# Kernel optimization log

Measured on AMD Instinct MI355X. Metric: run time of the kernel, lower is better.

Reference implementation:

```python
import jax, jax.numpy as jnp
import numpy as np

EMB_DIM = 1024
N_HEAD = 16
HEAD_DIM = EMB_DIM // N_HEAD


def setup_inputs() -> dict:
    key = jax.random.key(0)
    k1, k2, k3, k4, k5 = jax.random.split(key, 5)
    x = jax.random.normal(k1, (4, 2048, EMB_DIM), dtype=jnp.float32)
    s = 1.0 / np.sqrt(EMB_DIM)
    W_qkv = jax.random.uniform(k2, (3 * EMB_DIM, EMB_DIM), minval=-s, maxval=s, dtype=jnp.float32)
    b_qkv = jax.random.uniform(k3, (3 * EMB_DIM,), minval=-s, maxval=s, dtype=jnp.float32)
    W_proj = jax.random.uniform(k4, (EMB_DIM, EMB_DIM), minval=-s, maxval=s, dtype=jnp.float32)
    b_proj = jax.random.uniform(k5, (EMB_DIM,), minval=-s, maxval=s, dtype=jnp.float32)
    return {"x": x, "W_qkv": W_qkv, "b_qkv": b_qkv, "W_proj": W_proj, "b_proj": b_proj}


def reference(x, W_qkv, b_qkv, W_proj, b_proj):
    B, S, E = x.shape
    H, D = N_HEAD, HEAD_DIM
    qkv = x @ W_qkv.T + b_qkv  # [B,S,3E]
    q, k, v = jnp.split(qkv, 3, axis=-1)
    # [B,S,E] -> [B,H,S,D]
    q = q.reshape(B, S, H, D).transpose(0, 2, 1, 3)
    k = k.reshape(B, S, H, D).transpose(0, 2, 1, 3)
    v = v.reshape(B, S, H, D).transpose(0, 2, 1, 3)
    scale = 1.0 / jnp.sqrt(jnp.asarray(D, dtype=x.dtype))
    scores = jnp.einsum('bhqd,bhkd->bhqk', q, k) * scale
    causal = jnp.tril(jnp.ones((S, S), dtype=bool))
    scores = jnp.where(causal, scores, jnp.asarray(-jnp.inf, dtype=scores.dtype))
    attn = jax.nn.softmax(scores, axis=-1)
    y = jnp.einsum('bhqk,bhkd->bhqd', attn, v)  # [B,H,S,D]
    y = y.transpose(0, 2, 1, 3).reshape(B, S, E)
    return y @ W_proj.T + b_proj
```

## Files before the change

### kernel.cpp

```cpp
#include <hip/hip_runtime.h>
#include <hip/hip_bf16.h>

typedef __attribute__((ext_vector_type(4))) float f32x4;
typedef __attribute__((ext_vector_type(8))) __bf16 bf16x8;
typedef __attribute__((ext_vector_type(4))) unsigned int u32x4;

#define EMB 1024
#define NHEAD 16
#define HDIM 64
#define SEQ 2048
#define BATCH 4
#define NTOK 8192

__device__ __forceinline__ unsigned short f2bf(float f) {
    unsigned int u = __builtin_bit_cast(unsigned int, f);
    u = (u + 0x7fffu + ((u >> 16) & 1u)) >> 16;
    return (unsigned short)u;
}

__device__ __forceinline__ unsigned int pack_bf2(float lo, float hi) {
    unsigned int a = __builtin_bit_cast(unsigned int, lo);
    unsigned int b = __builtin_bit_cast(unsigned int, hi);
    return ((a + 0x8000u) >> 16) | ((b + 0x8000u) & 0xffff0000u);
}

__device__ __forceinline__ unsigned long long pack_bf4(const f32x4 v) {
    unsigned long long lo = pack_bf2(v[0], v[1]);
    unsigned long long hi = pack_bf2(v[2], v[3]);
    return (hi << 32) | lo;
}

__device__ __forceinline__ void async_copy16(const ushort* g, ushort* l) {
    __builtin_amdgcn_global_load_lds(
        (const __attribute__((address_space(1))) void*)g,
        (__attribute__((address_space(3))) void*)l,
        16, 0, 0);
}

__global__ void cvt_f32_bf16(const float4* __restrict__ in, ushort* __restrict__ out, int n4) {
    int i = blockIdx.x * 256 + threadIdx.x;
    if (i < n4) {
        float4 v = in[i];
        ushort4 o;
        o.x = f2bf(v.x); o.y = f2bf(v.y); o.z = f2bf(v.z); o.w = f2bf(v.w);
        ((ushort4*)out)[i] = o;
    }
}

#define GEMM_STAGE(Asrc, Bsrc, m0, n0, kt)                                        \
    {                                                                             \
        _Pragma("unroll")                                                         \
        for (int j = 0; j < 2; ++j) {                                             \
            int row = wave * 32 + j * 16 + (lane >> 2);                           \
            int kc  = (lane & 3) ^ ((row >> 1) & 3);                              \
            async_copy16(Asrc + (size_t)(m0 + row) * EMB + kt + kc * 8,           \
                         As + (wave * 32 + j * 16) * 32);                         \
            async_copy16(Bsrc + (size_t)(n0 + row) * EMB + kt + kc * 8,           \
                         Bs + (wave * 32 + j * 16) * 32);                         \
        }                                                                         \
    }

#define GEMM_BODY(Asrc, Bsrc, m0, n0)                                             \
    f32x4 acc[4][4] = {};                                                         \
    for (int kt = 0; kt < EMB; kt += 32) {                                        \
        GEMM_STAGE(Asrc, Bsrc, m0, n0, kt)                                        \
        __syncthreads();                                                          \
        bf16x8 a[4], b[4];                                                        \
        _Pragma("unroll")                                                         \
        for (int i = 0; i < 4; ++i) {                                             \
            int r = wm + i * 16 + col;                                            \
            a[i] = *(const bf16x8*)&As[r * 32 + (quad ^ ((r >> 1) & 3)) * 8];     \
            int c = wn + i * 16 + col;                                            \
            b[i] = *(const bf16x8*)&Bs[c * 32 + (quad ^ ((c >> 1) & 3)) * 8];     \
        }                                                                         \
        _Pragma("unroll")                                                         \
        for (int i = 0; i < 4; ++i)                                               \
            _Pragma("unroll")                                                     \
            for (int j = 0; j < 4; ++j)                                           \
                acc[i][j] = __builtin_amdgcn_mfma_f32_16x16x32_bf16(              \
                    a[i], b[j], acc[i][j], 0, 0, 0);                              \
        __syncthreads();                                                         \
    }

__global__ __launch_bounds__(256) void gemm_qk(
    const ushort* __restrict__ A,
    const ushort* __restrict__ W,
    const float*  __restrict__ bias,
    ushort* __restrict__ Qb, ushort* __restrict__ Kb)
{
    __shared__ ushort As[128 * 32];
    __shared__ ushort Bs[128 * 32];
    const int tid  = threadIdx.x;
    const int lane = tid & 63;
    const int wave = tid >> 6;
    const int col  = lane & 15;
    const int quad = lane >> 4;
    const int m0 = blockIdx.x * 128;
    const int n0 = blockIdx.y * 128;
    const int wm = (wave >> 1) * 64;
    const int wn = (wave & 1) * 64;

    GEMM_BODY(A, W, m0, n0)

    #pragma unroll
    for (int i = 0; i < 4; ++i)
        #pragma unroll
        for (int j = 0; j < 4; ++j)
            #pragma unroll
            for (int r = 0; r < 4; ++r) {
                int m = m0 + wm + i * 16 + quad * 4 + r;
                int n = n0 + wn + j * 16 + col;
                float v = acc[i][j][r] + bias[n];
                unsigned short bv = f2bf(v);
                int e = n & 1023;
                int h = e >> 6, d = e & 63;
                int b = m >> 11, s = m & 2047;
                size_t bh = (size_t)(b * NHEAD + h);
                if (n < 1024) Qb[(bh * SEQ + s) * HDIM + d] = bv;
                else          Kb[(bh * SEQ + s) * HDIM + d] = bv;
            }
}

__global__ __launch_bounds__(256) void gemm_vt(
    const ushort* __restrict__ Wv,
    const ushort* __restrict__ X,
    const float*  __restrict__ bias,
    ushort* __restrict__ Vtx)
{
    __shared__ ushort As[128 * 32];
    __shared__ ushort Bs[128 * 32];
    const int tid  = threadIdx.x;
    const int lane = tid & 63;
    const int wave = tid >> 6;
    const int col  = lane & 15;
    const int quad = lane >> 4;
    const int m0 = blockIdx.x * 128;
    const int n0 = blockIdx.y * 128;
    const int wm = (wave >> 1) * 64;
    const int wn = (wave & 1) * 64;

    GEMM_BODY(Wv, X, m0, n0)

    #pragma unroll
    for (int i = 0; i < 4; ++i)
        #pragma unroll
        for (int j = 0; j < 4; ++j)
            #pragma unroll
            for (int r = 0; r < 4; ++r) {
                int m = m0 + wm + i * 16 + quad * 4 + r;
                int n = n0 + wn + j * 16 + col;
                Vtx[(size_t)m * NTOK + n] = f2bf(acc[i][j][r] + bias[m]);
            }
}

__global__ __launch_bounds__(256) void gemm_proj(
    const ushort* __restrict__ A,
    const ushort* __restrict__ W,
    const float*  __restrict__ bias,
    float* __restrict__ out)
{
    __shared__ ushort As[128 * 32];
    __shared__ ushort Bs[128 * 32];
    const int tid  = threadIdx.x;
    const int lane = tid & 63;
    const int wave = tid >> 6;
    const int col  = lane & 15;
    const int quad = lane >> 4;
    const int m0 = blockIdx.x * 128;
    const int n0 = blockIdx.y * 128;
    const int wm = (wave >> 1) * 64;
    const int wn = (wave & 1) * 64;

    GEMM_BODY(A, W, m0, n0)

    #pragma unroll
    for (int i = 0; i < 4; ++i)
        #pragma unroll
        for (int j = 0; j < 4; ++j)
            #pragma unroll
            for (int r = 0; r < 4; ++r) {
                int m = m0 + wm + i * 16 + quad * 4 + r;
                int n = n0 + wn + j * 16 + col;
                out[(size_t)m * EMB + n] = acc[i][j][r] + bias[n];
            }
}

__device__ __forceinline__ void attn_qtile(
    int qb, int b, int h, int lane, int wave,
    const ushort* __restrict__ Qh, const ushort* __restrict__ Kh,
    const ushort* __restrict__ Vh, ushort* __restrict__ Yb,
    ushort* __restrict__ Ks0, ushort* __restrict__ Ks1, ushort* __restrict__ Vs,
    ushort* __restrict__ Ps)
{
    const int col  = lane & 15;
    const int quad = lane >> 4;
    const int q0  = qb * 64 + wave * 16;
    const int row = q0 + col;
    const float SC = 0.125f * 1.44269504f;

    bf16x8 qf0 = *(const bf16x8*)(Qh + (q0 + col) * HDIM + quad * 8);
    bf16x8 qf1 = *(const bf16x8*)(Qh + (q0 + col) * HDIM + 32 + quad * 8);

    ushort* Pw = Ps + wave * 2048;

    f32x4 o[4] = {};
    float lrun = 0.f;

    const int nk = (qb >> 1) + 1;
    for (int kt = 0; kt < nk; ++kt) {
        const int k0 = kt * 128;
        const bool last = (kt == nk - 1);

        {
            int srow = wave * 16 + (lane >> 2);
            #pragma unroll
            for (int rr = 0; rr < 2; ++rr) {
                int r = rr * 64 + srow;
                int kc = (lane & 3) ^ ((r >> 1) & 3);
                const ushort* src = Kh + (size_t)(k0 + r) * HDIM + kc * 8;
                async_copy16(src,      Ks0 + (rr * 64 + wave * 16) * 32);
                async_copy16(src + 32, Ks1 + (rr * 64 + wave * 16) * 32);
            }
            int kc = (lane & 3) ^ ((srow >> 1) & 3);
            const ushort* vsrc = Vh + (size_t)srow * NTOK + k0 + kc * 8;
            #pragma unroll
            for (int kq = 0; kq < 4; ++kq)
                async_copy16(vsrc + kq * 32, Vs + kq * 2048 + (wave * 16) * 32);
        }
        __syncthreads();

        f32x4 st[8];
        #pragma unroll
        for (int j = 0; j < 8; ++j) {
            int r = j * 16 + col;
            int q_ = (quad ^ ((r >> 1) & 3)) * 8;
            bf16x8 kf0 = *(const bf16x8*)&Ks0[r * 32 + q_];
            bf16x8 kf1 = *(const bf16x8*)&Ks1[r * 32 + q_];
            f32x4 z = {0.f, 0.f, 0.f, 0.f};
            st[j] = __builtin_amdgcn_mfma_f32_16x16x32_bf16(kf0, qf0, z, 0, 0, 0);
            st[j] = __builtin_amdgcn_mfma_f32_16x16x32_bf16(kf1, qf1, st[j], 0, 0, 0);
        }

        #pragma unroll
        for (int j = 0; j < 8; ++j)
            #pragma unroll
            for (int r = 0; r < 4; ++r) {
                float pv = exp2f(st[j][r] * SC);
                if (last) {
                    int c = k0 + j * 16 + quad * 4 + r;
                    pv = (c <= row) ? pv : 0.f;
                }
                st[j][r] = pv;
                lrun += pv;
            }

        #pragma unroll
        for (int j = 0; j < 8; ++j) {
            int blk = 2 * j + (quad >> 1);
            *(unsigned long long*)&Pw[col * 128 + ((blk ^ col) & 15) * 8 + (quad & 1) * 4]
                = pack_bf4(st[j]);
        }
        bf16x8 pf[4];
        #pragma unroll
        for (int kq = 0; kq < 4; ++kq) {
            int blk = 4 * kq + quad;
            pf[kq] = *(const bf16x8*)&Pw[col * 128 + ((blk ^ col) & 15) * 8];
        }

        #pragma unroll
        for (int dt = 0; dt < 4; ++dt) {
            int r = dt * 16 + col;
            int q_ = (quad ^ ((r >> 1) & 3)) * 8;
            #pragma unroll
            for (int kq = 0; kq < 4; ++kq) {
                bf16x8 vf = *(const bf16x8*)&Vs[kq * 2048 + r * 32 + q_];
                o[dt] = __builtin_amdgcn_mfma_f32_16x16x32_bf16(vf, pf[kq], o[dt], 0, 0, 0);
            }
        }
        __syncthreads();
    }

    lrun += __shfl_xor(lrun, 16, 64);
    lrun += __shfl_xor(lrun, 32, 64);
    float inv = 1.f / lrun;
    size_t rbase = ((size_t)(b * SEQ + row)) * EMB + h * HDIM + quad * 4;
    #pragma unroll
    for (int dt = 0; dt < 4; ++dt) {
        ushort4 s4;
        s4.x = f2bf(o[dt][0] * inv);
        s4.y = f2bf(o[dt][1] * inv);
        s4.z = f2bf(o[dt][2] * inv);
        s4.w = f2bf(o[dt][3] * inv);
        *(ushort4*)(Yb + rbase + dt * 16) = s4;
    }
}

__global__ __launch_bounds__(256, 4) void attn(
    const ushort* __restrict__ Qb, const ushort* __restrict__ Kb,
    const ushort* __restrict__ Vtx, ushort* __restrict__ Yb)
{
    __shared__ ushort Ks0[128 * 32];
    __shared__ ushort Ks1[128 * 32];
    __shared__ ushort Vs[4 * 64 * 32];
    __shared__ __align__(16) ushort Ps[4 * 2048];
    const int lane = threadIdx.x & 63;
    const int wave = threadIdx.x >> 6;
    const int bh   = blockIdx.x & 63;
    const int pr   = blockIdx.x >> 6;

    const int b = bh >> 4, h = bh & 15;
    const ushort* Qh = Qb + (size_t)bh * SEQ * HDIM;
    const ushort* Kh = Kb + (size_t)bh * SEQ * HDIM;
    const ushort* Vh = Vtx + (size_t)(h * HDIM) * NTOK + b * SEQ;

    attn_qtile(31 - pr, b, h, lane, wave, Qh, Kh, Vh, Yb, Ks0, Ks1, Vs, Ps);
    __syncthreads();
    attn_qtile(pr,      b, h, lane, wave, Qh, Kh, Vh, Yb, Ks0, Ks1, Vs, Ps);
}

extern "C" void kernel_launch(void* const* d_in, const int* in_sizes, int n_in,
                              void* d_out, int out_size, void* d_ws, size_t ws_size,
                              hipStream_t stream) {
    const float* x      = (const float*)d_in[0];
    const float* W_qkv  = (const float*)d_in[1];
    const float* b_qkv  = (const float*)d_in[2];
    const float* W_proj = (const float*)d_in[3];
    const float* b_proj = (const float*)d_in[4];
    float* out = (float*)d_out;

    ushort* ws     = (ushort*)d_ws;
    ushort* Xb     = ws;
    ushort* Yb     = ws;
    ushort* Wqkvb  = ws + 8388608;
    ushort* Wprojb = ws + 11534336;
    ushort* Qb     = ws + 12582912;
    ushort* Kb     = ws + 20971520;
    ushort* Vtx    = ws + 29360128;

    cvt_f32_bf16<<<8192, 256, 0, stream>>>((const float4*)x,      Xb,     2097152);
    cvt_f32_bf16<<<3072, 256, 0, stream>>>((const float4*)W_qkv,  Wqkvb,  786432);
    cvt_f32_bf16<<<1024, 256, 0, stream>>>((const float4*)W_proj, Wprojb, 262144);

    gemm_qk<<<dim3(64, 16), 256, 0, stream>>>(Xb, Wqkvb, b_qkv, Qb, Kb);
    gemm_vt<<<dim3(8, 64), 256, 0, stream>>>(Wqkvb + (size_t)2048 * EMB, Xb,
                                             b_qkv + 2048, Vtx);
    attn<<<1024, 256, 0, stream>>>(Qb, Kb, Vtx, Yb);
    gemm_proj<<<dim3(64, 8), 256, 0, stream>>>(Yb, Wprojb, b_proj, out);
}
```

Before: 282.7 us.

## Double-buffer K/V shared-memory tiles in causal attention loop

Splits the K/V tile load into a helper and allocates two LDS buffers each for K halves and V. The next key tile's async copy is issued before computing on the current tile, which removes one barrier per iteration and overlaps global loads with MFMA and softmax work. LDS per block grows from about 48KB to about 80KB, which can lower the number of resident blocks per CU. It also depends on the async copies having landed by the end-of-iteration barrier.

Result: no change. 280.7 us (-0.7%).

```diff
diff --git a/kernel.cpp b/kernel.cpp
--- a/kernel.cpp
+++ b/kernel.cpp
@@ -185,11 +185,35 @@
             }
 }
 
+__device__ __forceinline__ void attn_stage(
+    int k0, int lane, int wave,
+    const ushort* __restrict__ Kh, const ushort* __restrict__ Vh,
+    ushort* __restrict__ Ks0, ushort* __restrict__ Ks1, ushort* __restrict__ Vs)
+{
+    int srow = wave * 16 + (lane >> 2);
+    #pragma unroll
+    for (int rr = 0; rr < 2; ++rr) {
+        int r = rr * 64 + srow;
+        int kc = (lane & 3) ^ ((r >> 1) & 3);
+        const ushort* src = Kh + (size_t)(k0 + r) * HDIM + kc * 8;
+        async_copy16(src,      Ks0 + (rr * 64 + wave * 16) * 32);
+        async_copy16(src + 32, Ks1 + (rr * 64 + wave * 16) * 32);
+    }
+    int kc = (lane & 3) ^ ((srow >> 1) & 3);
+    const ushort* vsrc = Vh + (size_t)srow * NTOK + k0 + kc * 8;
+    #pragma unroll
+    for (int kq = 0; kq < 4; ++kq)
+        async_copy16(vsrc + kq * 32, Vs + kq * 2048 + (wave * 16) * 32);
+}
+
+#define KHALF 4096
+#define VBUF  8192
+
 __device__ __forceinline__ void attn_qtile(
     int qb, int b, int h, int lane, int wave,
     const ushort* __restrict__ Qh, const ushort* __restrict__ Kh,
     const ushort* __restrict__ Vh, ushort* __restrict__ Yb,
-    ushort* __restrict__ Ks0, ushort* __restrict__ Ks1, ushort* __restrict__ Vs,
+    ushort* __restrict__ Ks0b, ushort* __restrict__ Ks1b, ushort* __restrict__ Vsb,
     ushort* __restrict__ Ps)
 {
     const int col  = lane & 15;
@@ -207,35 +231,32 @@
     float lrun = 0.f;
 
     const int nk = (qb >> 1) + 1;
+
+    attn_stage(0, lane, wave, Kh, Vh, Ks0b, Ks1b, Vsb);
+    __syncthreads();
+
+    int cur = 0;
     for (int kt = 0; kt < nk; ++kt) {
         const int k0 = kt * 128;
         const bool last = (kt == nk - 1);
 
-        {
-            int srow = wave * 16 + (lane >> 2);
-            #pragma unroll
-            for (int rr = 0; rr < 2; ++rr) {
-                int r = rr * 64 + srow;
-                int kc = (lane & 3) ^ ((r >> 1) & 3);
-                const ushort* src = Kh + (size_t)(k0 + r) * HDIM + kc * 8;
-                async_copy16(src,      Ks0 + (rr * 64 + wave * 16) * 32);
-                async_copy16(src + 32, Ks1 + (rr * 64 + wave * 16) * 32);
-            }
-            int kc = (lane & 3) ^ ((srow >> 1) & 3);
-            const ushort* vsrc = Vh + (size_t)srow * NTOK + k0 + kc * 8;
-            #pragma unroll
-            for (int kq = 0; kq < 4; ++kq)
-                async_copy16(vsrc + kq * 32, Vs + kq * 2048 + (wave * 16) * 32);
-        }
-        __syncthreads();
+        if (!last)
+            attn_stage(k0 + 128, lane, wave, Kh, Vh,
+                       Ks0b + (cur ^ 1) * KHALF,
+                       Ks1b + (cur ^ 1) * KHALF,
+                       Vsb  + (cur ^ 1) * VBUF);
+
+        const ushort* K0c = Ks0b + cur * KHALF;
+        const ushort* K1c = Ks1b + cur * KHALF;
+        const ushort* Vc  = Vsb  + cur * VBUF;
 
         f32x4 st[8];
         #pragma unroll
         for (int j = 0; j < 8; ++j) {
             int r = j * 16 + col;
             int q_ = (quad ^ ((r >> 1) & 3)) * 8;
-            bf16x8 kf0 = *(const bf16x8*)&Ks0[r * 32 + q_];
-            bf16x8 kf1 = *(const bf16x8*)&Ks1[r * 32 + q_];
+            bf16x8 kf0 = *(const bf16x8*)&K0c[r * 32 + q_];
+            bf16x8 kf1 = *(const bf16x8*)&K1c[r * 32 + q_];
             f32x4 z = {0.f, 0.f, 0.f, 0.f};
             st[j] = __builtin_amdgcn_mfma_f32_16x16x32_bf16(kf0, qf0, z, 0, 0, 0);
             st[j] = __builtin_amdgcn_mfma_f32_16x16x32_bf16(kf1, qf1, st[j], 0, 0, 0);
@@ -273,11 +294,13 @@
             int q_ = (quad ^ ((r >> 1) & 3)) * 8;
             #pragma unroll
             for (int kq = 0; kq < 4; ++kq) {
-                bf16x8 vf = *(const bf16x8*)&Vs[kq * 2048 + r * 32 + q_];
+                bf16x8 vf = *(const bf16x8*)&Vc[kq * 2048 + r * 32 + q_];
                 o[dt] = __builtin_amdgcn_mfma_f32_16x16x32_bf16(vf, pf[kq], o[dt], 0, 0, 0);
             }
         }
+
         __syncthreads();
+        cur ^= 1;
     }
 
     lrun += __shfl_xor(lrun, 16, 64);
@@ -299,9 +322,9 @@
     const ushort* __restrict__ Qb, const ushort* __restrict__ Kb,
     const ushort* __restrict__ Vtx, ushort* __restrict__ Yb)
 {
-    __shared__ ushort Ks0[128 * 32];
-    __shared__ ushort Ks1[128 * 32];
-    __shared__ ushort Vs[4 * 64 * 32];
+    __shared__ ushort Ks0[2][128 * 32];
+    __shared__ ushort Ks1[2][128 * 32];
+    __shared__ ushort Vs[2][4 * 64 * 32];
     __shared__ __align__(16) ushort Ps[4 * 2048];
     const int lane = threadIdx.x & 63;
     const int wave = threadIdx.x >> 6;
@@ -313,9 +336,9 @@
     const ushort* Kh = Kb + (size_t)bh * SEQ * HDIM;
     const ushort* Vh = Vtx + (size_t)(h * HDIM) * NTOK + b * SEQ;
 
-    attn_qtile(31 - pr, b, h, lane, wave, Qh, Kh, Vh, Yb, Ks0, Ks1, Vs, Ps);
+    attn_qtile(31 - pr, b, h, lane, wave, Qh, Kh, Vh, Yb, Ks0[0], Ks1[0], Vs[0], Ps);
     __syncthreads();
-    attn_qtile(pr,      b, h, lane, wave, Qh, Kh, Vh, Yb, Ks0, Ks1, Vs, Ps);
+    attn_qtile(pr,      b, h, lane, wave, Qh, Kh, Vh, Yb, Ks0[0], Ks1[0], Vs[0], Ps);
 }
 
 extern "C" void kernel_launch(void* const* d_in, const int* in_sizes, int n_in,
```

## Load K and V fragments directly from global memory, dropping shared staging

Applied to the files above, without the earlier changes.

The attention kernel no longer stages K and V tiles into shared memory with async copies and block-wide barriers. Each wave now reads its MFMA operand fragments for K and V straight from global memory. This removes the LDS traffic and the two __syncthreads per key tile, and the lower LDS use may allow more blocks per CU. The cost is that all four waves redundantly fetch the same K/V data through the caches, using less coalesced 16-byte loads with exposed global latency.

Result: slower. 439.2 us (+55.3%).

```diff
diff --git a/kernel.cpp b/kernel.cpp
--- a/kernel.cpp
+++ b/kernel.cpp
@@ -189,7 +189,6 @@
     int qb, int b, int h, int lane, int wave,
     const ushort* __restrict__ Qh, const ushort* __restrict__ Kh,
     const ushort* __restrict__ Vh, ushort* __restrict__ Yb,
-    ushort* __restrict__ Ks0, ushort* __restrict__ Ks1, ushort* __restrict__ Vs,
     ushort* __restrict__ Ps)
 {
     const int col  = lane & 15;
@@ -211,31 +210,12 @@
         const int k0 = kt * 128;
         const bool last = (kt == nk - 1);
 
-        {
-            int srow = wave * 16 + (lane >> 2);
-            #pragma unroll
-            for (int rr = 0; rr < 2; ++rr) {
-                int r = rr * 64 + srow;
-                int kc = (lane & 3) ^ ((r >> 1) & 3);
-                const ushort* src = Kh + (size_t)(k0 + r) * HDIM + kc * 8;
-                async_copy16(src,      Ks0 + (rr * 64 + wave * 16) * 32);
-                async_copy16(src + 32, Ks1 + (rr * 64 + wave * 16) * 32);
-            }
-            int kc = (lane & 3) ^ ((srow >> 1) & 3);
-            const ushort* vsrc = Vh + (size_t)srow * NTOK + k0 + kc * 8;
-            #pragma unroll
-            for (int kq = 0; kq < 4; ++kq)
-                async_copy16(vsrc + kq * 32, Vs + kq * 2048 + (wave * 16) * 32);
-        }
-        __syncthreads();
-
+        const ushort* Kt = Kh + (size_t)(k0 + col) * HDIM + quad * 8;
         f32x4 st[8];
         #pragma unroll
         for (int j = 0; j < 8; ++j) {
-            int r = j * 16 + col;
-            int q_ = (quad ^ ((r >> 1) & 3)) * 8;
-            bf16x8 kf0 = *(const bf16x8*)&Ks0[r * 32 + q_];
-            bf16x8 kf1 = *(const bf16x8*)&Ks1[r * 32 + q_];
+            bf16x8 kf0 = *(const bf16x8*)(Kt + (size_t)(j * 16) * HDIM);
+            bf16x8 kf1 = *(const bf16x8*)(Kt + (size_t)(j * 16) * HDIM + 32);
             f32x4 z = {0.f, 0.f, 0.f, 0.f};
             st[j] = __builtin_amdgcn_mfma_f32_16x16x32_bf16(kf0, qf0, z, 0, 0, 0);
             st[j] = __builtin_amdgcn_mfma_f32_16x16x32_bf16(kf1, qf1, st[j], 0, 0, 0);
@@ -267,17 +247,16 @@
             pf[kq] = *(const bf16x8*)&Pw[col * 128 + ((blk ^ col) & 15) * 8];
         }
 
+        const ushort* Vt = Vh + (size_t)col * NTOK + k0 + quad * 8;
         #pragma unroll
         for (int dt = 0; dt < 4; ++dt) {
-            int r = dt * 16 + col;
-            int q_ = (quad ^ ((r >> 1) & 3)) * 8;
+            const ushort* Vr = Vt + (size_t)(dt * 16) * NTOK;
             #pragma unroll
             for (int kq = 0; kq < 4; ++kq) {
-                bf16x8 vf = *(const bf16x8*)&Vs[kq * 2048 + r * 32 + q_];
+                bf16x8 vf = *(const bf16x8*)(Vr + kq * 32);
                 o[dt] = __builtin_amdgcn_mfma_f32_16x16x32_bf16(vf, pf[kq], o[dt], 0, 0, 0);
             }
         }
-        __syncthreads();
     }
 
     lrun += __shfl_xor(lrun, 16, 64);
@@ -299,9 +278,6 @@
     const ushort* __restrict__ Qb, const ushort* __restrict__ Kb,
     const ushort* __restrict__ Vtx, ushort* __restrict__ Yb)
 {
-    __shared__ ushort Ks0[128 * 32];
-    __shared__ ushort Ks1[128 * 32];
-    __shared__ ushort Vs[4 * 64 * 32];
     __shared__ __align__(16) ushort Ps[4 * 2048];
     const int lane = threadIdx.x & 63;
     const int wave = threadIdx.x >> 6;
@@ -313,9 +289,8 @@
     const ushort* Kh = Kb + (size_t)bh * SEQ * HDIM;
     const ushort* Vh = Vtx + (size_t)(h * HDIM) * NTOK + b * SEQ;
 
-    attn_qtile(31 - pr, b, h, lane, wave, Qh, Kh, Vh, Yb, Ks0, Ks1, Vs, Ps);
-    __syncthreads();
-    attn_qtile(pr,      b, h, lane, wave, Qh, Kh, Vh, Yb, Ks0, Ks1, Vs, Ps);
+    attn_qtile(31 - pr, b, h, lane, wave, Qh, Kh, Vh, Yb, Ps);
+    attn_qtile(pr,      b, h, lane, wave, Qh, Kh, Vh, Yb, Ps);
 }
 
 extern "C" void kernel_launch(void* const* d_in, const int* in_sizes, int n_in,
```

## Enlarge attention query tile to 128 rows, two 16-row groups per wave

Applied to the files above, without the earlier changes.

Each wave now processes 32 query rows as two 16-row groups against the same staged K/V tile, which doubles the reuse of every K/V tile loaded into shared memory. Half as many blocks are launched, and each pairs query tile 15-pr with tile pr to balance the causal workload. The per-wave P buffer doubles and the launch bound drops to 2 blocks per SM, trading occupancy and registers for fewer K/V loads and fewer barriers per unit of work. The causal mask now falls on 128-wide diagonal tiles, so the last tile does more masked work.

Measured after the change: 269.5 us. 1.05x faster.

```diff
diff --git a/kernel.cpp b/kernel.cpp
--- a/kernel.cpp
+++ b/kernel.cpp
@@ -186,7 +186,7 @@
 }
 
 __device__ __forceinline__ void attn_qtile(
-    int qb, int b, int h, int lane, int wave,
+    int qt, int b, int h, int lane, int wave,
     const ushort* __restrict__ Qh, const ushort* __restrict__ Kh,
     const ushort* __restrict__ Vh, ushort* __restrict__ Yb,
     ushort* __restrict__ Ks0, ushort* __restrict__ Ks1, ushort* __restrict__ Vs,
@@ -194,19 +194,23 @@
 {
     const int col  = lane & 15;
     const int quad = lane >> 4;
-    const int q0  = qb * 64 + wave * 16;
-    const int row = q0 + col;
+    const int q0   = qt * 128 + wave * 32;
     const float SC = 0.125f * 1.44269504f;
 
-    bf16x8 qf0 = *(const bf16x8*)(Qh + (q0 + col) * HDIM + quad * 8);
-    bf16x8 qf1 = *(const bf16x8*)(Qh + (q0 + col) * HDIM + 32 + quad * 8);
-
-    ushort* Pw = Ps + wave * 2048;
-
-    f32x4 o[4] = {};
-    float lrun = 0.f;
-
-    const int nk = (qb >> 1) + 1;
+    bf16x8 qf[2][2];
+    #pragma unroll
+    for (int g = 0; g < 2; ++g) {
+        const ushort* qp = Qh + (size_t)(q0 + g * 16 + col) * HDIM;
+        qf[g][0] = *(const bf16x8*)(qp + quad * 8);
+        qf[g][1] = *(const bf16x8*)(qp + 32 + quad * 8);
+    }
+
+    ushort* Pw = Ps + wave * 4096;
+
+    f32x4 o[2][4] = {};
+    float lrun[2] = {0.f, 0.f};
+
+    const int nk = qt + 1;
     for (int kt = 0; kt < nk; ++kt) {
         const int k0 = kt * 128;
         const bool last = (kt == nk - 1);
@@ -229,43 +233,56 @@
         }
         __syncthreads();
 
-        f32x4 st[8];
+        f32x4 st[2][8];
         #pragma unroll
         for (int j = 0; j < 8; ++j) {
             int r = j * 16 + col;
             int q_ = (quad ^ ((r >> 1) & 3)) * 8;
             bf16x8 kf0 = *(const bf16x8*)&Ks0[r * 32 + q_];
             bf16x8 kf1 = *(const bf16x8*)&Ks1[r * 32 + q_];
-            f32x4 z = {0.f, 0.f, 0.f, 0.f};
-            st[j] = __builtin_amdgcn_mfma_f32_16x16x32_bf16(kf0, qf0, z, 0, 0, 0);
-            st[j] = __builtin_amdgcn_mfma_f32_16x16x32_bf16(kf1, qf1, st[j], 0, 0, 0);
-        }
-
-        #pragma unroll
-        for (int j = 0; j < 8; ++j)
-            #pragma unroll
-            for (int r = 0; r < 4; ++r) {
-                float pv = exp2f(st[j][r] * SC);
-                if (last) {
-                    int c = k0 + j * 16 + quad * 4 + r;
-                    pv = (c <= row) ? pv : 0.f;
+            #pragma unroll
+            for (int g = 0; g < 2; ++g) {
+                f32x4 z = {0.f, 0.f, 0.f, 0.f};
+                f32x4 t = __builtin_amdgcn_mfma_f32_16x16x32_bf16(kf0, qf[g][0], z, 0, 0, 0);
+                st[g][j] = __builtin_amdgcn_mfma_f32_16x16x32_bf16(kf1, qf[g][1], t, 0, 0, 0);
+            }
+        }
+
+        #pragma unroll
+        for (int g = 0; g < 2; ++g) {
+            int rowg = q0 + g * 16 + col;
+            #pragma unroll
+            for (int j = 0; j < 8; ++j)
+                #pragma unroll
+                for (int r = 0; r < 4; ++r) {
+                    float pv = exp2f(st[g][j][r] * SC);
+                    if (last) {
+                        int c = k0 + j * 16 + quad * 4 + r;
+                        pv = (c <= rowg) ? pv : 0.f;
+                    }
+                    st[g][j][r] = pv;
+                    lrun[g] += pv;
                 }
-                st[j][r] = pv;
-                lrun += pv;
-            }
-
-        #pragma unroll
-        for (int j = 0; j < 8; ++j) {
-            int blk = 2 * j + (quad >> 1);
-            *(unsigned long long*)&Pw[col * 128 + ((blk ^ col) & 15) * 8 + (quad & 1) * 4]
-                = pack_bf4(st[j]);
-        }
-        bf16x8 pf[4];
-        #pragma unroll
-        for (int kq = 0; kq < 4; ++kq) {
-            int blk = 4 * kq + quad;
-            pf[kq] = *(const bf16x8*)&Pw[col * 128 + ((blk ^ col) & 15) * 8];
-        }
+        }
+
+        #pragma unroll
+        for (int g = 0; g < 2; ++g)
+            #pragma unroll
+            for (int j = 0; j < 8; ++j) {
+                int blk = 2 * j + (quad >> 1);
+                *(unsigned long long*)&Pw[g * 2048 + col * 128 +
+                                          ((blk ^ col) & 15) * 8 + (quad & 1) * 4]
+                    = pack_bf4(st[g][j]);
+            }
+        bf16x8 pf[2][4];
+        #pragma unroll
+        for (int g = 0; g < 2; ++g)
+            #pragma unroll
+            for (int kq = 0; kq < 4; ++kq) {
+                int blk = 4 * kq + quad;
+                pf[g][kq] = *(const bf16x8*)&Pw[g * 2048 + col * 128 +
+                                                ((blk ^ col) & 15) * 8];
+            }
 
         #pragma unroll
         for (int dt = 0; dt < 4; ++dt) {
@@ -274,35 +291,41 @@
             #pragma unroll
             for (int kq = 0; kq < 4; ++kq) {
                 bf16x8 vf = *(const bf16x8*)&Vs[kq * 2048 + r * 32 + q_];
-                o[dt] = __builtin_amdgcn_mfma_f32_16x16x32_bf16(vf, pf[kq], o[dt], 0, 0, 0);
+                o[0][dt] = __builtin_amdgcn_mfma_f32_16x16x32_bf16(vf, pf[0][kq], o[0][dt], 0, 0, 0);
+                o[1][dt] = __builtin_amdgcn_mfma_f32_16x16x32_bf16(vf, pf[1][kq], o[1][dt], 0, 0, 0);
             }
         }
         __syncthreads();
     }
 
-    lrun += __shfl_xor(lrun, 16, 64);
-    lrun += __shfl_xor(lrun, 32, 64);
-    float inv = 1.f / lrun;
-    size_t rbase = ((size_t)(b * SEQ + row)) * EMB + h * HDIM + quad * 4;
-    #pragma unroll
-    for (int dt = 0; dt < 4; ++dt) {
-        ushort4 s4;
-        s4.x = f2bf(o[dt][0] * inv);
-        s4.y = f2bf(o[dt][1] * inv);
-        s4.z = f2bf(o[dt][2] * inv);
-        s4.w = f2bf(o[dt][3] * inv);
-        *(ushort4*)(Yb + rbase + dt * 16) = s4;
-    }
-}
-
-__global__ __launch_bounds__(256, 4) void attn(
+    #pragma unroll
+    for (int g = 0; g < 2; ++g) {
+        float l = lrun[g];
+        l += __shfl_xor(l, 16, 64);
+        l += __shfl_xor(l, 32, 64);
+        float inv = 1.f / l;
+        int rowg = q0 + g * 16 + col;
+        size_t rbase = ((size_t)(b * SEQ + rowg)) * EMB + h * HDIM + quad * 4;
+        #pragma unroll
+        for (int dt = 0; dt < 4; ++dt) {
+            ushort4 s4;
+            s4.x = f2bf(o[g][dt][0] * inv);
+            s4.y = f2bf(o[g][dt][1] * inv);
+            s4.z = f2bf(o[g][dt][2] * inv);
+            s4.w = f2bf(o[g][dt][3] * inv);
+            *(ushort4*)(Yb + rbase + dt * 16) = s4;
+        }
+    }
+}
+
+__global__ __launch_bounds__(256, 2) void attn(
     const ushort* __restrict__ Qb, const ushort* __restrict__ Kb,
     const ushort* __restrict__ Vtx, ushort* __restrict__ Yb)
 {
     __shared__ ushort Ks0[128 * 32];
     __shared__ ushort Ks1[128 * 32];
     __shared__ ushort Vs[4 * 64 * 32];
-    __shared__ __align__(16) ushort Ps[4 * 2048];
+    __shared__ __align__(16) ushort Ps[4 * 4096];
     const int lane = threadIdx.x & 63;
     const int wave = threadIdx.x >> 6;
     const int bh   = blockIdx.x & 63;
@@ -313,7 +336,7 @@
     const ushort* Kh = Kb + (size_t)bh * SEQ * HDIM;
     const ushort* Vh = Vtx + (size_t)(h * HDIM) * NTOK + b * SEQ;
 
-    attn_qtile(31 - pr, b, h, lane, wave, Qh, Kh, Vh, Yb, Ks0, Ks1, Vs, Ps);
+    attn_qtile(15 - pr, b, h, lane, wave, Qh, Kh, Vh, Yb, Ks0, Ks1, Vs, Ps);
     __syncthreads();
     attn_qtile(pr,      b, h, lane, wave, Qh, Kh, Vh, Yb, Ks0, Ks1, Vs, Ps);
 }
@@ -344,6 +367,6 @@
     gemm_qk<<<dim3(64, 16), 256, 0, stream>>>(Xb, Wqkvb, b_qkv, Qb, Kb);
     gemm_vt<<<dim3(8, 64), 256, 0, stream>>>(Wqkvb + (size_t)2048 * EMB, Xb,
                                              b_qkv + 2048, Vtx);
-    attn<<<1024, 256, 0, stream>>>(Qb, Kb, Vtx, Yb);
+    attn<<<512, 256, 0, stream>>>(Qb, Kb, Vtx, Yb);
     gemm_proj<<<dim3(64, 8), 256, 0, stream>>>(Yb, Wprojb, b_proj, out);
 }
```
